# Performance work log

Hardware: AMD Instinct MI355X
Metric: run time of the kernel (lower is better)

Reference implementation:

```python
import jax, jax.numpy as jnp
import numpy as np
import math

NEG_INF = float(np.finfo(np.float32).min)
EPS = 1e-6
N_MIX = 8

def setup_inputs() -> dict:
    key = jax.random.key(0)
    ks = jax.random.split(key, 9)
    B, KMAX, KDIM, QDIM, VDIM = 32, 2048, 512, 512, 512
    return {
        "key_feat": jax.random.normal(ks[0], (B, KMAX, KDIM), jnp.float32),
        "value": jax.random.normal(ks[1], (B, KMAX, VDIM), jnp.float32),
        "query": jax.random.normal(ks[2], (B, 1, QDIM), jnp.float32),
        "mask": jnp.ones((B, KMAX), jnp.int32),
        "W_gamma": jax.random.normal(ks[3], (N_MIX, QDIM), jnp.float32) * (1.0 / math.sqrt(QDIM)),
        "b_gamma": jnp.zeros((N_MIX,), jnp.float32),
        "W_beta": jax.random.normal(ks[4], (N_MIX, QDIM), jnp.float32) * (1.0 / math.sqrt(QDIM)),
        "b_beta": jnp.zeros((N_MIX,), jnp.float32),
        "W_kappa": jax.random.normal(ks[5], (N_MIX, QDIM), jnp.float32) * (1.0 / math.sqrt(QDIM)),
        "b_kappa": jnp.zeros((N_MIX,), jnp.float32),
    }

def reference(key_feat, value, query, mask, W_gamma, b_gamma, W_beta, b_beta, W_kappa, b_kappa):
    B, kmax = key_feat.shape[:2]
    # per-step linear projections of query [B,1,qdim] -> [B,1,n_mix]
    w = jax.nn.softmax(jnp.einsum('bsq,mq->bsm', query, W_gamma) + b_gamma, axis=-1)
    v = jnp.exp(jnp.einsum('bsq,mq->bsm', query, W_beta) + b_beta)
    # myu_prev is zeros on the first decoding step (self.myu is None)
    myu = jnp.exp(jnp.einsum('bsq,mq->bsm', query, W_kappa) + b_kappa)
    # positions js: [1, kmax, 1] broadcast against [B, 1, n_mix]
    js = jnp.arange(kmax, dtype=jnp.float32)[None, :, None]
    numerator = jnp.exp(-jnp.square(js - myu) / (2.0 * v + EPS))
    denominator = jnp.sqrt(2.0 * math.pi * v + EPS)
    aw = jnp.sum(w * numerator / denominator, axis=2)  # [B, kmax]
    aw = jnp.where(mask == 0, NEG_INF, aw)
    cv = jnp.einsum('bk,bkd->bd', aw, value)[:, None, :]  # [B, 1, value_dim]
    return cv, aw[:, :, None]
```

## Files before the change

kernel.cpp:

```cpp
#include <hip/hip_runtime.h>
#include <math.h>

#define BB    32
#define KMAX  2048
#define QDIM  512
#define VDIM  512
#define NMIX  8
#define EPSV  1e-6f
#define NEGINF -3.40282347e38f
#define TWO_PI 6.28318530717958647692f

__global__ void gmm_proj_kernel(const float* __restrict__ query,
                                const float* __restrict__ Wg, const float* __restrict__ bg,
                                const float* __restrict__ Wb, const float* __restrict__ bb,
                                const float* __restrict__ Wk, const float* __restrict__ bk,
                                float* __restrict__ params)
{
    int b = blockIdx.x;
    int t = threadIdx.x;
    int wave = t >> 6, lane = t & 63;
    __shared__ float dots[24];

    const float4* q4 = (const float4*)(query + (size_t)b * QDIM);
    for (int j = wave; j < 24; j += 4) {
        int set = j >> 3, m = j & 7;
        const float* Wrow = (set == 0 ? Wg : (set == 1 ? Wb : Wk)) + (size_t)m * QDIM;
        const float4* W4 = (const float4*)Wrow;
        float s = 0.f;
        for (int d = lane; d < QDIM / 4; d += 64) {
            float4 a = q4[d], w = W4[d];
            s += a.x * w.x + a.y * w.y + a.z * w.z + a.w * w.w;
        }
        #pragma unroll
        for (int off = 32; off; off >>= 1) s += __shfl_down(s, off, 64);
        if (lane == 0) dots[j] = s;
    }
    __syncthreads();

    if (t == 0) {
        float g[8], mx = -1e30f;
        #pragma unroll
        for (int m = 0; m < 8; m++) { g[m] = dots[m] + bg[m]; mx = fmaxf(mx, g[m]); }
        float sum = 0.f;
        #pragma unroll
        for (int m = 0; m < 8; m++) { g[m] = expf(g[m] - mx); sum += g[m]; }
        float inv_sum = 1.f / sum;
        float* p = params + b * 24;
        #pragma unroll
        for (int m = 0; m < 8; m++) {
            float w   = g[m] * inv_sum;
            float v   = expf(dots[8 + m]  + bb[m]);
            float myu = expf(dots[16 + m] + bk[m]);
            p[m]      = myu;
            p[8 + m]  = 1.f / (2.f * v + EPSV);
            p[16 + m] = w * rsqrtf(TWO_PI * v + EPSV);
        }
    }
}

__global__ void gmm_aw_cv_partial_kernel(const float* __restrict__ value,
                                         const int*   __restrict__ mask,
                                         const float* __restrict__ params,
                                         float* __restrict__ aw_out,
                                         float* __restrict__ partial,
                                         int nsplit, int kchunk)
{
    int b = blockIdx.x / nsplit;
    int s = blockIdx.x % nsplit;
    int t = threadIdx.x;
    __shared__ float aw_s[256];

    const float* p = params + b * 24;
    int k0 = s * kchunk;

    for (int k = t; k < kchunk; k += 128) {
        float j = (float)(k0 + k);
        float aw = 0.f;
        #pragma unroll
        for (int m = 0; m < 8; m++) {
            float d = j - p[m];
            aw += p[16 + m] * expf(-d * d * p[8 + m]);
        }
        if (mask[(size_t)b * KMAX + k0 + k] == 0) aw = NEGINF;
        aw_s[k] = aw;
        aw_out[(size_t)b * KMAX + k0 + k] = aw;
    }
    __syncthreads();

    const float4* vb = (const float4*)(value + ((size_t)b * KMAX + k0) * VDIM);
    float4 acc = make_float4(0.f, 0.f, 0.f, 0.f);
    #pragma unroll 4
    for (int kk = 0; kk < kchunk; kk++) {
        float a = aw_s[kk];
        float4 v = vb[(size_t)kk * (VDIM / 4) + t];
        acc.x += a * v.x; acc.y += a * v.y; acc.z += a * v.z; acc.w += a * v.w;
    }
    ((float4*)(partial + ((size_t)b * nsplit + s) * VDIM))[t] = acc;
}

__global__ void gmm_reduce_kernel(const float* __restrict__ partial,
                                  float* __restrict__ cv, int nsplit)
{
    int idx = blockIdx.x * blockDim.x + threadIdx.x;
    int b = idx >> 9;
    int d = idx & 511;
    const float* p = partial + (size_t)b * nsplit * VDIM + d;
    float sum = 0.f;
    for (int i = 0; i < nsplit; i++) sum += p[(size_t)i * VDIM];
    cv[idx] = sum;
}

extern "C" void kernel_launch(void* const* d_in, const int* in_sizes, int n_in,
                              void* d_out, int out_size, void* d_ws, size_t ws_size,
                              hipStream_t stream) {
    const float* value = (const float*)d_in[1];
    const float* query = (const float*)d_in[2];
    const int*   mask  = (const int*)d_in[3];
    const float* Wg = (const float*)d_in[4];
    const float* bg = (const float*)d_in[5];
    const float* Wb = (const float*)d_in[6];
    const float* bb = (const float*)d_in[7];
    const float* Wk = (const float*)d_in[8];
    const float* bk = (const float*)d_in[9];

    float* out = (float*)d_out;
    float* cv  = out;
    float* aw  = out + BB * VDIM;

    float* params  = (float*)d_ws;
    float* partial = params + BB * 24;

    int nsplit = 64;
    while (nsplit > 8 &&
           (size_t)(BB * 24 + (size_t)BB * nsplit * VDIM) * sizeof(float) > ws_size)
        nsplit >>= 1;
    int kchunk = KMAX / nsplit;

    gmm_proj_kernel<<<BB, 256, 0, stream>>>(query, Wg, bg, Wb, bb, Wk, bk, params);
    gmm_aw_cv_partial_kernel<<<BB * nsplit, 128, 0, stream>>>(
        value, mask, params, aw, partial, nsplit, kchunk);
    gmm_reduce_kernel<<<(BB * VDIM) / 256, 256, 0, stream>>>(partial, cv, nsplit);
}
```

Before: 283.3 us.

## Fuse projection, attention weights and value reduction into one kernel with atomics

Merges the three kernels into a single kernel. Each block recomputes the query projection for its batch row, then computes its chunk of attention weights and the partial context vector. Partials are accumulated into the output with atomicAdd after a memset, which removes the workspace round trip and two launches. The cost is redundant projection work in every block (64x per batch), atomic contention, and a summation order that is no longer deterministic.

```diff
diff --git a/kernel.cpp b/kernel.cpp
--- a/kernel.cpp
+++ b/kernel.cpp
@@ -1,39 +1,50 @@
 #include <hip/hip_runtime.h>
 #include <math.h>
 
-#define BB    32
-#define KMAX  2048
-#define QDIM  512
-#define VDIM  512
-#define NMIX  8
-#define EPSV  1e-6f
+#define BB     32
+#define KMAX   2048
+#define QDIM   512
+#define VDIM   512
+#define NMIX   8
+#define EPSV   1e-6f
 #define NEGINF -3.40282347e38f
 #define TWO_PI 6.28318530717958647692f
+#define NSPLIT 64
+#define KCHUNK (KMAX / NSPLIT)
 
-__global__ void gmm_proj_kernel(const float* __restrict__ query,
-                                const float* __restrict__ Wg, const float* __restrict__ bg,
-                                const float* __restrict__ Wb, const float* __restrict__ bb,
-                                const float* __restrict__ Wk, const float* __restrict__ bk,
-                                float* __restrict__ params)
+__global__ __launch_bounds__(128) void gmm_fused_kernel(
+    const float* __restrict__ value,
+    const float* __restrict__ query,
+    const int*   __restrict__ mask,
+    const float* __restrict__ Wg, const float* __restrict__ bg,
+    const float* __restrict__ Wb, const float* __restrict__ bb,
+    const float* __restrict__ Wk, const float* __restrict__ bk,
+    float* __restrict__ cv,
+    float* __restrict__ aw_out)
 {
-    int b = blockIdx.x;
-    int t = threadIdx.x;
+    int blk  = blockIdx.x;
+    int b    = blk >> 6;
+    int s    = blk & (NSPLIT - 1);
+    int t    = threadIdx.x;
     int wave = t >> 6, lane = t & 63;
+
     __shared__ float dots[24];
+    __shared__ float p[24];
+    __shared__ float aw_s[KCHUNK];
 
     const float4* q4 = (const float4*)(query + (size_t)b * QDIM);
-    for (int j = wave; j < 24; j += 4) {
+    float4 a0 = q4[lane];
+    float4 a1 = q4[lane + 64];
+    for (int j = wave; j < 24; j += 2) {
         int set = j >> 3, m = j & 7;
         const float* Wrow = (set == 0 ? Wg : (set == 1 ? Wb : Wk)) + (size_t)m * QDIM;
         const float4* W4 = (const float4*)Wrow;
-        float s = 0.f;
-        for (int d = lane; d < QDIM / 4; d += 64) {
-            float4 a = q4[d], w = W4[d];
-            s += a.x * w.x + a.y * w.y + a.z * w.z + a.w * w.w;
-        }
+        float4 w0 = W4[lane], w1 = W4[lane + 64];
+        float ss = a0.x * w0.x + a0.y * w0.y + a0.z * w0.z + a0.w * w0.w
+                 + a1.x * w1.x + a1.y * w1.y + a1.z * w1.z + a1.w * w1.w;
         #pragma unroll
-        for (int off = 32; off; off >>= 1) s += __shfl_down(s, off, 64);
-        if (lane == 0) dots[j] = s;
+        for (int off = 32; off; off >>= 1) ss += __shfl_down(ss, off, 64);
+        if (lane == 0) dots[j] = ss;
     }
     __syncthreads();
 
@@ -45,7 +56,6 @@
         #pragma unroll
         for (int m = 0; m < 8; m++) { g[m] = expf(g[m] - mx); sum += g[m]; }
         float inv_sum = 1.f / sum;
-        float* p = params + b * 24;
         #pragma unroll
         for (int m = 0; m < 8; m++) {
             float w   = g[m] * inv_sum;
@@ -56,58 +66,37 @@
             p[16 + m] = w * rsqrtf(TWO_PI * v + EPSV);
         }
     }
-}
+    __syncthreads();
 
-__global__ void gmm_aw_cv_partial_kernel(const float* __restrict__ value,
-                                         const int*   __restrict__ mask,
-                                         const float* __restrict__ params,
-                                         float* __restrict__ aw_out,
-                                         float* __restrict__ partial,
-                                         int nsplit, int kchunk)
-{
-    int b = blockIdx.x / nsplit;
-    int s = blockIdx.x % nsplit;
-    int t = threadIdx.x;
-    __shared__ float aw_s[256];
-
-    const float* p = params + b * 24;
-    int k0 = s * kchunk;
-
-    for (int k = t; k < kchunk; k += 128) {
-        float j = (float)(k0 + k);
+    int k0 = s * KCHUNK;
+    if (t < KCHUNK) {
+        int k = k0 + t;
+        float j = (float)k;
         float aw = 0.f;
         #pragma unroll
         for (int m = 0; m < 8; m++) {
             float d = j - p[m];
             aw += p[16 + m] * expf(-d * d * p[8 + m]);
         }
-        if (mask[(size_t)b * KMAX + k0 + k] == 0) aw = NEGINF;
-        aw_s[k] = aw;
-        aw_out[(size_t)b * KMAX + k0 + k] = aw;
+        if (mask[(size_t)b * KMAX + k] == 0) aw = NEGINF;
+        aw_s[t] = aw;
+        aw_out[(size_t)b * KMAX + k] = aw;
     }
     __syncthreads();
 
     const float4* vb = (const float4*)(value + ((size_t)b * KMAX + k0) * VDIM);
     float4 acc = make_float4(0.f, 0.f, 0.f, 0.f);
-    #pragma unroll 4
-    for (int kk = 0; kk < kchunk; kk++) {
+    #pragma unroll 8
+    for (int kk = 0; kk < KCHUNK; kk++) {
         float a = aw_s[kk];
         float4 v = vb[(size_t)kk * (VDIM / 4) + t];
         acc.x += a * v.x; acc.y += a * v.y; acc.z += a * v.z; acc.w += a * v.w;
     }
-    ((float4*)(partial + ((size_t)b * nsplit + s) * VDIM))[t] = acc;
-}
-
-__global__ void gmm_reduce_kernel(const float* __restrict__ partial,
-                                  float* __restrict__ cv, int nsplit)
-{
-    int idx = blockIdx.x * blockDim.x + threadIdx.x;
-    int b = idx >> 9;
-    int d = idx & 511;
-    const float* p = partial + (size_t)b * nsplit * VDIM + d;
-    float sum = 0.f;
-    for (int i = 0; i < nsplit; i++) sum += p[(size_t)i * VDIM];
-    cv[idx] = sum;
+    float* cvp = cv + (size_t)b * VDIM + t * 4;
+    atomicAdd(cvp + 0, acc.x);
+    atomicAdd(cvp + 1, acc.y);
+    atomicAdd(cvp + 2, acc.z);
+    atomicAdd(cvp + 3, acc.w);
 }
 
 extern "C" void kernel_launch(void* const* d_in, const int* in_sizes, int n_in,
@@ -127,17 +116,8 @@
     float* cv  = out;
     float* aw  = out + BB * VDIM;
 
-    float* params  = (float*)d_ws;
-    float* partial = params + BB * 24;
+    hipMemsetAsync(cv, 0, (size_t)BB * VDIM * sizeof(float), stream);
 
-    int nsplit = 64;
-    while (nsplit > 8 &&
-           (size_t)(BB * 24 + (size_t)BB * nsplit * VDIM) * sizeof(float) > ws_size)
-        nsplit >>= 1;
-    int kchunk = KMAX / nsplit;
-
-    gmm_proj_kernel<<<BB, 256, 0, stream>>>(query, Wg, bg, Wb, bb, Wk, bk, params);
-    gmm_aw_cv_partial_kernel<<<BB * nsplit, 128, 0, stream>>>(
-        value, mask, params, aw, partial, nsplit, kchunk);
-    gmm_reduce_kernel<<<(BB * VDIM) / 256, 256, 0, stream>>>(partial, cv, nsplit);
+    gmm_fused_kernel<<<BB * NSPLIT, 128, 0, stream>>>(
+        value, query, mask, Wg, bg, Wb, bb, Wk, bk, cv, aw);
 }
```

New measurement: 270.2 us. -4.6%, faster.
